# Optimization experiments

Hardware: AMD Instinct MI355X
Metric: run time of the kernel (lower is better)

Reference implementation:

```python
import jax, jax.numpy as jnp
import numpy as np

B, L, D, H = 2, 2048, 1024, 16
HD = D // H  # head_dim = 64


def setup_inputs() -> dict:
    key = jax.random.key(0)
    ks = jax.random.split(key, 8)
    queries = jax.random.normal(ks[0], (B, L, D), dtype=jnp.float32)
    keys = jax.random.normal(ks[1], (B, L, D), dtype=jnp.float32)
    values = jax.random.normal(ks[2], (B, L, D), dtype=jnp.float32)
    mask = jax.random.randint(ks[3], (B, L, L), 0, 2) > 0  # True = masked
    s = 1.0 / np.sqrt(D)
    W_q = jax.random.normal(ks[4], (D, D), dtype=jnp.float32) * s
    W_k = jax.random.normal(ks[5], (D, D), dtype=jnp.float32) * s
    W_v = jax.random.normal(ks[6], (D, D), dtype=jnp.float32) * s
    W_o = jax.random.normal(ks[7], (D, D), dtype=jnp.float32) * s
    return {"queries": queries, "keys": keys, "values": values,
            "W_q": W_q, "W_k": W_k, "W_v": W_v, "W_o": W_o, "mask": mask}


def _split_heads(x):
    # [B, L, D] -> [B, H, L, HD]
    return x.reshape(B, L, H, HD).transpose(0, 2, 1, 3)


def reference(queries, keys, values, W_q, W_k, W_v, W_o, mask):
    # Linear projections (nn.Linear: x @ W.T, no bias)
    q = _split_heads(queries @ W_q.T)   # [B,H,Lq,HD]
    k = _split_heads(keys @ W_k.T)      # [B,H,Lk,HD]
    v = _split_heads(values @ W_v.T)    # [B,H,Lk,HD]
    scores = jnp.einsum('bnqd,bnkd->bnqk', q, k) / np.sqrt(HD)
    scores = jnp.where(mask[:, None, :, :], -1e9, scores)
    attn = jax.nn.softmax(scores, axis=-1)
    ctx = jnp.einsum('bnqk,bnkd->bnqd', attn, v)
    ctx = ctx.transpose(0, 2, 1, 3).reshape(B, L, D)
    return ctx @ W_o.T  # dropout p=0.0 -> identity
```

## Files before the change

kernel.cpp:

```cpp
#include <hip/hip_runtime.h>
#include <hip/hip_bf16.h>

typedef __bf16 bf16;
typedef __attribute__((ext_vector_type(8))) __bf16 bf16x8;
typedef __attribute__((ext_vector_type(4))) __bf16 bf16x4;
typedef __attribute__((ext_vector_type(4))) float f32x4;

#define B_   2
#define L_   2048
#define D_   1024
#define H_   16
#define HD_  64

__device__ __forceinline__ void gll16(const bf16* g, bf16* l) {
  __builtin_amdgcn_global_load_lds((const __attribute__((address_space(1))) void*)g,
                                   (__attribute__((address_space(3))) void*)l,
                                   16, 0, 0);
}

__global__ void detect_kernel(const unsigned short* __restrict__ q_u,
                              const unsigned char* __restrict__ m_u,
                              int* __restrict__ flags) {
  __shared__ int cnt, odd;
  if (threadIdx.x == 0) { cnt = 0; odd = 0; }
  __syncthreads();
  int c = 0, o = 0;
  for (int i = 0; i < 32; i++) {
    int idx = threadIdx.x * 32 + i;
    unsigned e = (q_u[idx] >> 7) & 0xFF;
    if (e >= 0x8F || (e > 0 && e <= 0x6F)) c++;
    if ((idx & 3) && m_u[idx]) o = 1;
  }
  atomicAdd(&cnt, c);
  if (o) atomicOr(&odd, 1);
  __syncthreads();
  if (threadIdx.x == 0) { flags[0] = (cnt > 512) ? 1 : 0; flags[1] = odd; }
}

__device__ __forceinline__ void canon_body(const void* src, bf16* dst, int i, int f) {
  if (f) {
    const float4* s = (const float4*)src;
    float4 a = s[i / 4], b2 = s[i / 4 + 1];
    bf16x8 o;
    o[0] = (bf16)a.x;  o[1] = (bf16)a.y;  o[2] = (bf16)a.z;  o[3] = (bf16)a.w;
    o[4] = (bf16)b2.x; o[5] = (bf16)b2.y; o[6] = (bf16)b2.z; o[7] = (bf16)b2.w;
    *(bf16x8*)(dst + i) = o;
  } else {
    *(bf16x8*)(dst + i) = ((const bf16x8*)src)[i / 8];
  }
}

__global__ __launch_bounds__(256) void canon_all(
    const void* xq, const void* xk, const void* xv,
    const void* Wq, const void* Wk, const void* Wv, const void* Wo,
    bf16* cxq, bf16* cxk, bf16* cxv,
    bf16* cWq, bf16* cWk, bf16* cWv, bf16* cWo,
    const int* __restrict__ flags) {
  const int f = flags[0];
  int t = blockIdx.x;
  const void* src; bf16* dst; int base;
  if (t < 2048)      { src = xq; dst = cxq; base = t * 2048; }
  else if (t < 4096) { src = xk; dst = cxk; base = (t - 2048) * 2048; }
  else if (t < 6144) { src = xv; dst = cxv; base = (t - 4096) * 2048; }
  else {
    int w = t - 6144, wi = w >> 9;
    base = (w & 511) * 2048;
    if (wi == 0)      { src = Wq; dst = cWq; }
    else if (wi == 1) { src = Wk; dst = cWk; }
    else if (wi == 2) { src = Wv; dst = cWv; }
    else              { src = Wo; dst = cWo; }
  }
  canon_body(src, dst, base + threadIdx.x * 8, f);
}

__global__ __launch_bounds__(256) void pack_mask(const void* __restrict__ mp,
                                                 const int* __restrict__ flags,
                                                 unsigned* __restrict__ bitsT) {
  int wid = blockIdx.x * 256 + threadIdx.x;
  unsigned v = 0;
  if (flags[1]) {
    const uchar4* p = (const uchar4*)mp;
#pragma unroll
    for (int c = 0; c < 8; c++) {
      uchar4 u = p[wid * 8 + c];
      v |= (u.x ? 1u : 0u) << (c * 4 + 0);
      v |= (u.y ? 1u : 0u) << (c * 4 + 1);
      v |= (u.z ? 1u : 0u) << (c * 4 + 2);
      v |= (u.w ? 1u : 0u) << (c * 4 + 3);
    }
  } else {
    const int4* p = (const int4*)mp;
#pragma unroll
    for (int c = 0; c < 8; c++) {
      int4 u = p[wid * 8 + c];
      v |= (u.x ? 1u : 0u) << (c * 4 + 0);
      v |= (u.y ? 1u : 0u) << (c * 4 + 1);
      v |= (u.z ? 1u : 0u) << (c * 4 + 2);
      v |= (u.w ? 1u : 0u) << (c * 4 + 3);
    }
  }
  int row = wid >> 6, word = wid & 63;
  int kt = word >> 1, half = word & 1;
  bitsT[((size_t)kt * 4096 + row) * 2 + half] = v;
}

__global__ __launch_bounds__(256) void gemm_qkv(
    const bf16* __restrict__ Aq, const bf16* __restrict__ Bq, bf16* __restrict__ Cq,
    const bf16* __restrict__ Ak, const bf16* __restrict__ Bk, bf16* __restrict__ Ck,
    const bf16* __restrict__ Av, const bf16* __restrict__ Bv, bf16* __restrict__ VT) {
  __shared__ bf16 smem[64 * 136];
  bf16* sA = smem;
  bf16* sB = smem + 4096;
  const int z = blockIdx.z;
  const bf16* A  = (z == 0) ? Aq : (z == 1) ? Ak : Av;
  const bf16* Bm = (z == 0) ? Bq : (z == 1) ? Bk : Bv;

  const int tid = threadIdx.x;
  const int w = tid >> 6, lane = tid & 63, qd = lane >> 4, r = lane & 15;
  const int wm = w >> 1, wn = w & 1;
  const int m0 = blockIdx.x * 128, n0 = blockIdx.y * 64;

  f32x4 acc[4][2];
#pragma unroll
  for (int i = 0; i < 4; i++)
#pragma unroll
    for (int j = 0; j < 2; j++) acc[i][j] = (f32x4){0.f, 0.f, 0.f, 0.f};

  for (int k0 = 0; k0 < 1024; k0 += 32) {
    __syncthreads();
    {
      int c0 = tid;
      gll16(A + (size_t)(m0 + (c0 >> 2)) * 1024 + k0 + (c0 & 3) * 8, sA + c0 * 8);
      int c1 = 256 + tid;
      gll16(A + (size_t)(m0 + (c1 >> 2)) * 1024 + k0 + (c1 & 3) * 8, sA + c1 * 8);
      int cb = tid;
      gll16(Bm + (size_t)(n0 + (cb >> 2)) * 1024 + k0 + (cb & 3) * 8, sB + cb * 8);
    }
    __syncthreads();
    bf16x8 af[4], bfv[2];
#pragma unroll
    for (int i = 0; i < 4; i++)
      af[i] = *(const bf16x8*)&sA[(wm * 64 + i * 16 + r) * 32 + qd * 8];
#pragma unroll
    for (int j = 0; j < 2; j++)
      bfv[j] = *(const bf16x8*)&sB[(wn * 32 + j * 16 + r) * 32 + qd * 8];
#pragma unroll
    for (int i = 0; i < 4; i++)
#pragma unroll
      for (int j = 0; j < 2; j++)
        acc[i][j] = __builtin_amdgcn_mfma_f32_16x16x32_bf16(af[i], bfv[j], acc[i][j], 0, 0, 0);
  }

  if (z < 2) {
    bf16* C = (z == 0) ? Cq : Ck;
#pragma unroll
    for (int i = 0; i < 4; i++)
#pragma unroll
      for (int j = 0; j < 2; j++)
#pragma unroll
        for (int rr = 0; rr < 4; rr++) {
          int row = m0 + wm * 64 + i * 16 + qd * 4 + rr;
          int col = n0 + wn * 32 + j * 16 + r;
          C[(size_t)row * 1024 + col] = (bf16)acc[i][j][rr];
        }
  } else {
    __syncthreads();
#pragma unroll
    for (int i = 0; i < 4; i++)
#pragma unroll
      for (int j = 0; j < 2; j++) {
        int col = wn * 32 + j * 16 + r;
        int rowb = wm * 64 + i * 16 + qd * 4;
        bf16x4 v4;
#pragma unroll
        for (int rr = 0; rr < 4; rr++) v4[rr] = (bf16)acc[i][j][rr];
        *(bf16x4*)&smem[col * 136 + rowb] = v4;
      }
    __syncthreads();
    const int b = m0 >> 11, tok0 = m0 & 2047, h = n0 >> 6;
    const int bh = b * 16 + h;
#pragma unroll
    for (int p = 0; p < 4; p++) {
      int c = p * 256 + tid;
      int d = c >> 4, ch = c & 15;
      bf16x8 v = *(const bf16x8*)&smem[d * 136 + ch * 8];
      *(bf16x8*)(VT + ((size_t)(bh * 64 + d)) * 2048 + tok0 + ch * 8) = v;
    }
  }
}

__global__ __launch_bounds__(256) void gemm_nt_out(const bf16* __restrict__ A,
                                                   const bf16* __restrict__ Bm,
                                                   void* __restrict__ Cout,
                                                   const int* __restrict__ flags) {
  __shared__ bf16 sA[128 * 32];
  __shared__ bf16 sB[64 * 32];
  const int tid = threadIdx.x;
  const int w = tid >> 6, lane = tid & 63, qd = lane >> 4, r = lane & 15;
  const int wm = w >> 1, wn = w & 1;
  const int m0 = blockIdx.x * 128, n0 = blockIdx.y * 64;

  f32x4 acc[4][2];
#pragma unroll
  for (int i = 0; i < 4; i++)
#pragma unroll
    for (int j = 0; j < 2; j++) acc[i][j] = (f32x4){0.f, 0.f, 0.f, 0.f};

  for (int k0 = 0; k0 < 1024; k0 += 32) {
    __syncthreads();
    {
      int c0 = tid;
      gll16(A + (size_t)(m0 + (c0 >> 2)) * 1024 + k0 + (c0 & 3) * 8, sA + c0 * 8);
      int c1 = 256 + tid;
      gll16(A + (size_t)(m0 + (c1 >> 2)) * 1024 + k0 + (c1 & 3) * 8, sA + c1 * 8);
      int cb = tid;
      gll16(Bm + (size_t)(n0 + (cb >> 2)) * 1024 + k0 + (cb & 3) * 8, sB + cb * 8);
    }
    __syncthreads();
    bf16x8 af[4], bfv[2];
#pragma unroll
    for (int i = 0; i < 4; i++)
      af[i] = *(const bf16x8*)&sA[(wm * 64 + i * 16 + r) * 32 + qd * 8];
#pragma unroll
    for (int j = 0; j < 2; j++)
      bfv[j] = *(const bf16x8*)&sB[(wn * 32 + j * 16 + r) * 32 + qd * 8];
#pragma unroll
    for (int i = 0; i < 4; i++)
#pragma unroll
      for (int j = 0; j < 2; j++)
        acc[i][j] = __builtin_amdgcn_mfma_f32_16x16x32_bf16(af[i], bfv[j], acc[i][j], 0, 0, 0);
  }
  const int f = flags[0];
#pragma unroll
  for (int i = 0; i < 4; i++)
#pragma unroll
    for (int j = 0; j < 2; j++)
#pragma unroll
      for (int rr = 0; rr < 4; rr++) {
        int row = m0 + wm * 64 + i * 16 + qd * 4 + rr;
        int col = n0 + wn * 32 + j * 16 + r;
        if (f) ((float*)Cout)[(size_t)row * 1024 + col] = acc[i][j][rr];
        else   ((bf16*)Cout)[(size_t)row * 1024 + col] = (bf16)acc[i][j][rr];
      }
}

__global__ __launch_bounds__(256) void attn_kernel(const bf16* __restrict__ Q,
                                                   const bf16* __restrict__ Kp,
                                                   const bf16* __restrict__ Vt,
                                                   const unsigned* __restrict__ bitsT,
                                                   bf16* __restrict__ CTX) {
  __shared__ bf16 sK[64 * 64];
  __shared__ bf16 sVT[64 * 64];
  __shared__ bf16 sP[128 * 72];
  const int tid = threadIdx.x;
  const int w = tid >> 6, lane = tid & 63, qd = lane >> 4, r = lane & 15;
  const int bh = blockIdx.y, b = bh >> 4, h = bh & 15;
  const int q0 = blockIdx.x * 128;

  bf16x8 qf[2][2];
#pragma unroll
  for (int i = 0; i < 2; i++)
#pragma unroll
    for (int ks = 0; ks < 2; ks++)
      qf[i][ks] = *(const bf16x8*)(Q + (size_t)(b * L_ + q0 + w * 32 + i * 16 + r) * D_ +
                                   h * HD_ + ks * 32 + qd * 8);

  bf16x8 ones;
#pragma unroll
  for (int e = 0; e < 8; e++) ones[e] = (bf16)1.0f;

  f32x4 o[2][4], lacc[2];
#pragma unroll
  for (int i = 0; i < 2; i++) {
#pragma unroll
    for (int dj = 0; dj < 4; dj++) o[i][dj] = (f32x4){0.f, 0.f, 0.f, 0.f};
    lacc[i] = (f32x4){0.f, 0.f, 0.f, 0.f};
  }

  for (int kt = 0; kt < L_ / 64; kt++) {
    __syncthreads();
#pragma unroll
    for (int p = 0; p < 2; p++) {
      int c = p * 256 + tid;
      int row = c >> 3, kc = c & 7;
      int kcg = kc ^ (row & 7);
      gll16(Kp + (size_t)(b * L_ + kt * 64 + row) * D_ + h * HD_ + kcg * 8, sK + c * 8);
    }
#pragma unroll
    for (int p = 0; p < 2; p++) {
      int c = p * 256 + tid;
      int row = c >> 3, kc = c & 7;
      int kcg = kc ^ (row & 7);
      gll16(Vt + (size_t)(bh * 64 + row) * L_ + kt * 64 + kcg * 8, sVT + c * 8);
    }
    __syncthreads();

    uint4 mq[2][2];
#pragma unroll
    for (int i = 0; i < 2; i++) {
      const uint4* mp4 = (const uint4*)(bitsT +
          ((size_t)kt * 4096 + b * 2048 + q0 + w * 32 + i * 16 + qd * 4) * 2);
      mq[i][0] = mp4[0];
      mq[i][1] = mp4[1];
    }

    bf16x8 kf[4][2];
#pragma unroll
    for (int j = 0; j < 4; j++)
#pragma unroll
      for (int ks = 0; ks < 2; ks++) {
        int row = j * 16 + r;
        int phys = (ks * 4 + qd) ^ (row & 7);
        kf[j][ks] = *(const bf16x8*)&sK[row * 64 + phys * 8];
      }

#pragma unroll
    for (int i = 0; i < 2; i++) {
      f32x4 S[4];
#pragma unroll
      for (int j = 0; j < 4; j++) {
        S[j] = (f32x4){0.f, 0.f, 0.f, 0.f};
#pragma unroll
        for (int ks = 0; ks < 2; ks++)
          S[j] = __builtin_amdgcn_mfma_f32_16x16x32_bf16(qf[i][ks], kf[j][ks], S[j], 0, 0, 0);
      }
#pragma unroll
      for (int j = 0; j < 4; j++)
#pragma unroll
        for (int rr = 0; rr < 4; rr++) {
          unsigned w32;
          if (rr == 0) w32 = (j < 2) ? mq[i][0].x : mq[i][0].y;
          else if (rr == 1) w32 = (j < 2) ? mq[i][0].z : mq[i][0].w;
          else if (rr == 2) w32 = (j < 2) ? mq[i][1].x : mq[i][1].y;
          else w32 = (j < 2) ? mq[i][1].z : mq[i][1].w;
          float e = __expf(S[j][rr] * 0.125f);
          bool msk = (w32 >> ((j & 1) * 16 + r)) & 1u;
          sP[(w * 32 + i * 16 + qd * 4 + rr) * 72 + j * 16 + r] = (bf16)(msk ? 0.f : e);
        }
    }
    asm volatile("s_waitcnt lgkmcnt(0)" ::: "memory");

    bf16x8 vf[4][2];
#pragma unroll
    for (int dj = 0; dj < 4; dj++)
#pragma unroll
      for (int ks = 0; ks < 2; ks++) {
        int row = dj * 16 + r;
        int phys = (ks * 4 + qd) ^ (row & 7);
        vf[dj][ks] = *(const bf16x8*)&sVT[row * 64 + phys * 8];
      }
#pragma unroll
    for (int i = 0; i < 2; i++)
#pragma unroll
      for (int ks = 0; ks < 2; ks++) {
        bf16x8 pf = *(const bf16x8*)&sP[(w * 32 + i * 16 + r) * 72 + ks * 32 + qd * 8];
#pragma unroll
        for (int dj = 0; dj < 4; dj++)
          o[i][dj] = __builtin_amdgcn_mfma_f32_16x16x32_bf16(pf, vf[dj][ks], o[i][dj], 0, 0, 0);
        lacc[i] = __builtin_amdgcn_mfma_f32_16x16x32_bf16(pf, ones, lacc[i], 0, 0, 0);
      }
  }

#pragma unroll
  for (int i = 0; i < 2; i++) {
    float inv[4];
#pragma unroll
    for (int rr = 0; rr < 4; rr++) inv[rr] = 1.0f / lacc[i][rr];
#pragma unroll
    for (int dj = 0; dj < 4; dj++)
#pragma unroll
      for (int rr = 0; rr < 4; rr++) {
        int row = b * L_ + q0 + w * 32 + i * 16 + qd * 4 + rr;
        int col = h * HD_ + dj * 16 + r;
        CTX[(size_t)row * D_ + col] = (bf16)(o[i][dj][rr] * inv[rr]);
      }
  }
}

extern "C" void kernel_launch(void* const* d_in, const int* in_sizes, int n_in,
                              void* d_out, int out_size, void* d_ws, size_t ws_size,
                              hipStream_t stream) {
  const void* xq = d_in[0];
  const void* xk = d_in[1];
  const void* xv = d_in[2];
  const void* Wq = d_in[3];
  const void* Wk = d_in[4];
  const void* Wv = d_in[5];
  const void* Wo = d_in[6];
  const void* mask = d_in[7];

  char* ws = (char*)d_ws;
  const size_t MB = 1048576;
  int*      FLAGS = (int*)(ws + 0);
  unsigned* BITS  = (unsigned*)(ws + 4096);
  bf16* cWq = (bf16*)(ws + 2 * MB);
  bf16* cWk = (bf16*)(ws + 4 * MB);
  bf16* cWv = (bf16*)(ws + 6 * MB);
  bf16* cWo = (bf16*)(ws + 8 * MB);
  bf16* cxq = (bf16*)(ws + 10 * MB);
  bf16* cxk = (bf16*)(ws + 18 * MB);
  bf16* cxv = (bf16*)(ws + 26 * MB);
  bf16* Q   = (bf16*)(ws + 34 * MB);
  bf16* K   = (bf16*)(ws + 42 * MB);
  bf16* VT  = (bf16*)(ws + 50 * MB);
  bf16* CTX = cxq;

  detect_kernel<<<1, 256, 0, stream>>>((const unsigned short*)xq,
                                       (const unsigned char*)mask, FLAGS);
  canon_all<<<8192, 256, 0, stream>>>(xq, xk, xv, Wq, Wk, Wv, Wo,
                                      cxq, cxk, cxv, cWq, cWk, cWv, cWo, FLAGS);
  pack_mask<<<1024, 256, 0, stream>>>(mask, FLAGS, BITS);
  gemm_qkv<<<dim3(32, 16, 3), 256, 0, stream>>>(cxq, cWq, Q,
                                                cxk, cWk, K,
                                                cxv, cWv, VT);
  attn_kernel<<<dim3(16, 32), 256, 0, stream>>>(Q, K, VT, BITS, CTX);
  gemm_nt_out<<<dim3(32, 16), 256, 0, stream>>>(CTX, cWo, d_out, FLAGS);
}
```

Before: 285.6 us.

## Split attention over key range, widen GEMM tiles, fold softmax scale into Q

The attention kernel is split into two key halves via a grid z dimension, writing unnormalized partial outputs and row sums that a new combine kernel adds and normalizes. This doubles the number of attention blocks for more parallelism, at the cost of an extra kernel and extra memory traffic. The QKV and output GEMMs move from 128x64 to 128x128 tiles for more reuse per block. The 1/8 scale and log2(e) factor are folded into Q at projection time so the softmax can use a raw exp2. There is no running max, which is safe only if the scores stay bounded.

```diff
diff --git a/kernel.cpp b/kernel.cpp
--- a/kernel.cpp
+++ b/kernel.cpp
@@ -11,6 +11,18 @@
 #define D_   1024
 #define H_   16
 #define HD_  64
+
+__device__ __forceinline__ float fast_exp2(float x) {
+#if defined(__has_builtin)
+#if __has_builtin(__builtin_amdgcn_exp2f)
+  return __builtin_amdgcn_exp2f(x);
+#else
+  float e; asm("v_exp_f32 %0, %1" : "=v"(e) : "v"(x)); return e;
+#endif
+#else
+  float e; asm("v_exp_f32 %0, %1" : "=v"(e) : "v"(x)); return e;
+#endif
+}
 
 __device__ __forceinline__ void gll16(const bf16* g, bf16* l) {
   __builtin_amdgcn_global_load_lds((const __attribute__((address_space(1))) void*)g,
@@ -108,7 +120,7 @@
     const bf16* __restrict__ Aq, const bf16* __restrict__ Bq, bf16* __restrict__ Cq,
     const bf16* __restrict__ Ak, const bf16* __restrict__ Bk, bf16* __restrict__ Ck,
     const bf16* __restrict__ Av, const bf16* __restrict__ Bv, bf16* __restrict__ VT) {
-  __shared__ bf16 smem[64 * 136];
+  __shared__ bf16 smem[128 * 136];
   bf16* sA = smem;
   bf16* sB = smem + 4096;
   const int z = blockIdx.z;
@@ -118,58 +130,61 @@
   const int tid = threadIdx.x;
   const int w = tid >> 6, lane = tid & 63, qd = lane >> 4, r = lane & 15;
   const int wm = w >> 1, wn = w & 1;
-  const int m0 = blockIdx.x * 128, n0 = blockIdx.y * 64;
-
-  f32x4 acc[4][2];
+  const int m0 = blockIdx.x * 128, n0 = blockIdx.y * 128;
+
+  f32x4 acc[4][4];
 #pragma unroll
   for (int i = 0; i < 4; i++)
 #pragma unroll
-    for (int j = 0; j < 2; j++) acc[i][j] = (f32x4){0.f, 0.f, 0.f, 0.f};
+    for (int j = 0; j < 4; j++) acc[i][j] = (f32x4){0.f, 0.f, 0.f, 0.f};
 
   for (int k0 = 0; k0 < 1024; k0 += 32) {
     __syncthreads();
-    {
-      int c0 = tid;
-      gll16(A + (size_t)(m0 + (c0 >> 2)) * 1024 + k0 + (c0 & 3) * 8, sA + c0 * 8);
-      int c1 = 256 + tid;
-      gll16(A + (size_t)(m0 + (c1 >> 2)) * 1024 + k0 + (c1 & 3) * 8, sA + c1 * 8);
-      int cb = tid;
-      gll16(Bm + (size_t)(n0 + (cb >> 2)) * 1024 + k0 + (cb & 3) * 8, sB + cb * 8);
-    }
-    __syncthreads();
-    bf16x8 af[4], bfv[2];
+#pragma unroll
+    for (int p = 0; p < 2; p++) {
+      int c = p * 256 + tid;
+      gll16(A + (size_t)(m0 + (c >> 2)) * 1024 + k0 + (c & 3) * 8, sA + c * 8);
+    }
+#pragma unroll
+    for (int p = 0; p < 2; p++) {
+      int c = p * 256 + tid;
+      gll16(Bm + (size_t)(n0 + (c >> 2)) * 1024 + k0 + (c & 3) * 8, sB + c * 8);
+    }
+    __syncthreads();
+    bf16x8 af[4], bfv[4];
 #pragma unroll
     for (int i = 0; i < 4; i++)
       af[i] = *(const bf16x8*)&sA[(wm * 64 + i * 16 + r) * 32 + qd * 8];
 #pragma unroll
-    for (int j = 0; j < 2; j++)
-      bfv[j] = *(const bf16x8*)&sB[(wn * 32 + j * 16 + r) * 32 + qd * 8];
-#pragma unroll
-    for (int i = 0; i < 4; i++)
-#pragma unroll
-      for (int j = 0; j < 2; j++)
+    for (int j = 0; j < 4; j++)
+      bfv[j] = *(const bf16x8*)&sB[(wn * 64 + j * 16 + r) * 32 + qd * 8];
+#pragma unroll
+    for (int i = 0; i < 4; i++)
+#pragma unroll
+      for (int j = 0; j < 4; j++)
         acc[i][j] = __builtin_amdgcn_mfma_f32_16x16x32_bf16(af[i], bfv[j], acc[i][j], 0, 0, 0);
   }
 
   if (z < 2) {
     bf16* C = (z == 0) ? Cq : Ck;
-#pragma unroll
-    for (int i = 0; i < 4; i++)
-#pragma unroll
-      for (int j = 0; j < 2; j++)
+    const float s = (z == 0) ? 0.1803368801f : 1.0f;
+#pragma unroll
+    for (int i = 0; i < 4; i++)
+#pragma unroll
+      for (int j = 0; j < 4; j++)
 #pragma unroll
         for (int rr = 0; rr < 4; rr++) {
           int row = m0 + wm * 64 + i * 16 + qd * 4 + rr;
-          int col = n0 + wn * 32 + j * 16 + r;
-          C[(size_t)row * 1024 + col] = (bf16)acc[i][j][rr];
+          int col = n0 + wn * 64 + j * 16 + r;
+          C[(size_t)row * 1024 + col] = (bf16)(acc[i][j][rr] * s);
         }
   } else {
     __syncthreads();
 #pragma unroll
     for (int i = 0; i < 4; i++)
 #pragma unroll
-      for (int j = 0; j < 2; j++) {
-        int col = wn * 32 + j * 16 + r;
+      for (int j = 0; j < 4; j++) {
+        int col = wn * 64 + j * 16 + r;
         int rowb = wm * 64 + i * 16 + qd * 4;
         bf16x4 v4;
 #pragma unroll
@@ -177,14 +192,14 @@
         *(bf16x4*)&smem[col * 136 + rowb] = v4;
       }
     __syncthreads();
-    const int b = m0 >> 11, tok0 = m0 & 2047, h = n0 >> 6;
-    const int bh = b * 16 + h;
-#pragma unroll
-    for (int p = 0; p < 4; p++) {
-      int c = p * 256 + tid;
-      int d = c >> 4, ch = c & 15;
-      bf16x8 v = *(const bf16x8*)&smem[d * 136 + ch * 8];
-      *(bf16x8*)(VT + ((size_t)(bh * 64 + d)) * 2048 + tok0 + ch * 8) = v;
+    const int b = m0 >> 11, tok0 = m0 & 2047, h0 = n0 >> 6;
+#pragma unroll
+    for (int p = 0; p < 8; p++) {
+      int c = p * 256 + tid;
+      int dl = c >> 4, ch = c & 15;
+      bf16x8 v = *(const bf16x8*)&smem[dl * 136 + ch * 8];
+      int head = h0 + (dl >> 6), d = dl & 63;
+      *(bf16x8*)(VT + ((size_t)((b * 16 + head) * 64 + d)) * 2048 + tok0 + ch * 8) = v;
     }
   }
 }
@@ -194,51 +209,53 @@
                                                    void* __restrict__ Cout,
                                                    const int* __restrict__ flags) {
   __shared__ bf16 sA[128 * 32];
-  __shared__ bf16 sB[64 * 32];
+  __shared__ bf16 sB[128 * 32];
   const int tid = threadIdx.x;
   const int w = tid >> 6, lane = tid & 63, qd = lane >> 4, r = lane & 15;
   const int wm = w >> 1, wn = w & 1;
-  const int m0 = blockIdx.x * 128, n0 = blockIdx.y * 64;
-
-  f32x4 acc[4][2];
+  const int m0 = blockIdx.x * 128, n0 = blockIdx.y * 128;
+
+  f32x4 acc[4][4];
 #pragma unroll
   for (int i = 0; i < 4; i++)
 #pragma unroll
-    for (int j = 0; j < 2; j++) acc[i][j] = (f32x4){0.f, 0.f, 0.f, 0.f};
+    for (int j = 0; j < 4; j++) acc[i][j] = (f32x4){0.f, 0.f, 0.f, 0.f};
 
   for (int k0 = 0; k0 < 1024; k0 += 32) {
     __syncthreads();
-    {
-      int c0 = tid;
-      gll16(A + (size_t)(m0 + (c0 >> 2)) * 1024 + k0 + (c0 & 3) * 8, sA + c0 * 8);
-      int c1 = 256 + tid;
-      gll16(A + (size_t)(m0 + (c1 >> 2)) * 1024 + k0 + (c1 & 3) * 8, sA + c1 * 8);
-      int cb = tid;
-      gll16(Bm + (size_t)(n0 + (cb >> 2)) * 1024 + k0 + (cb & 3) * 8, sB + cb * 8);
-    }
-    __syncthreads();
-    bf16x8 af[4], bfv[2];
+#pragma unroll
+    for (int p = 0; p < 2; p++) {
+      int c = p * 256 + tid;
+      gll16(A + (size_t)(m0 + (c >> 2)) * 1024 + k0 + (c & 3) * 8, sA + c * 8);
+    }
+#pragma unroll
+    for (int p = 0; p < 2; p++) {
+      int c = p * 256 + tid;
+      gll16(Bm + (size_t)(n0 + (c >> 2)) * 1024 + k0 + (c & 3) * 8, sB + c * 8);
+    }
+    __syncthreads();
+    bf16x8 af[4], bfv[4];
 #pragma unroll
     for (int i = 0; i < 4; i++)
       af[i] = *(const bf16x8*)&sA[(wm * 64 + i * 16 + r) * 32 + qd * 8];
 #pragma unroll
-    for (int j = 0; j < 2; j++)
-      bfv[j] = *(const bf16x8*)&sB[(wn * 32 + j * 16 + r) * 32 + qd * 8];
-#pragma unroll
-    for (int i = 0; i < 4; i++)
-#pragma unroll
-      for (int j = 0; j < 2; j++)
+    for (int j = 0; j < 4; j++)
+      bfv[j] = *(const bf16x8*)&sB[(wn * 64 + j * 16 + r) * 32 + qd * 8];
+#pragma unroll
+    for (int i = 0; i < 4; i++)
+#pragma unroll
+      for (int j = 0; j < 4; j++)
         acc[i][j] = __builtin_amdgcn_mfma_f32_16x16x32_bf16(af[i], bfv[j], acc[i][j], 0, 0, 0);
   }
   const int f = flags[0];
 #pragma unroll
   for (int i = 0; i < 4; i++)
 #pragma unroll
-    for (int j = 0; j < 2; j++)
+    for (int j = 0; j < 4; j++)
 #pragma unroll
       for (int rr = 0; rr < 4; rr++) {
         int row = m0 + wm * 64 + i * 16 + qd * 4 + rr;
-        int col = n0 + wn * 32 + j * 16 + r;
+        int col = n0 + wn * 64 + j * 16 + r;
         if (f) ((float*)Cout)[(size_t)row * 1024 + col] = acc[i][j][rr];
         else   ((bf16*)Cout)[(size_t)row * 1024 + col] = (bf16)acc[i][j][rr];
       }
@@ -248,7 +265,8 @@
                                                    const bf16* __restrict__ Kp,
                                                    const bf16* __restrict__ Vt,
                                                    const unsigned* __restrict__ bitsT,
-                                                   bf16* __restrict__ CTX) {
+                                                   bf16* __restrict__ OP,
+                                                   float* __restrict__ LP) {
   __shared__ bf16 sK[64 * 64];
   __shared__ bf16 sVT[64 * 64];
   __shared__ bf16 sP[128 * 72];
@@ -256,6 +274,7 @@
   const int w = tid >> 6, lane = tid & 63, qd = lane >> 4, r = lane & 15;
   const int bh = blockIdx.y, b = bh >> 4, h = bh & 15;
   const int q0 = blockIdx.x * 128;
+  const int z = blockIdx.z;
 
   bf16x8 qf[2][2];
 #pragma unroll
@@ -277,7 +296,7 @@
     lacc[i] = (f32x4){0.f, 0.f, 0.f, 0.f};
   }
 
-  for (int kt = 0; kt < L_ / 64; kt++) {
+  for (int kt = z * 16; kt < z * 16 + 16; kt++) {
     __syncthreads();
 #pragma unroll
     for (int p = 0; p < 2; p++) {
@@ -333,7 +352,7 @@
           else if (rr == 1) w32 = (j < 2) ? mq[i][0].z : mq[i][0].w;
           else if (rr == 2) w32 = (j < 2) ? mq[i][1].x : mq[i][1].y;
           else w32 = (j < 2) ? mq[i][1].z : mq[i][1].w;
-          float e = __expf(S[j][rr] * 0.125f);
+          float e = fast_exp2(S[j][rr]);
           bool msk = (w32 >> ((j & 1) * 16 + r)) & 1u;
           sP[(w * 32 + i * 16 + qd * 4 + rr) * 72 + j * 16 + r] = (bf16)(msk ? 0.f : e);
         }
@@ -363,18 +382,38 @@
 
 #pragma unroll
   for (int i = 0; i < 2; i++) {
-    float inv[4];
-#pragma unroll
-    for (int rr = 0; rr < 4; rr++) inv[rr] = 1.0f / lacc[i][rr];
 #pragma unroll
     for (int dj = 0; dj < 4; dj++)
 #pragma unroll
       for (int rr = 0; rr < 4; rr++) {
-        int row = b * L_ + q0 + w * 32 + i * 16 + qd * 4 + rr;
+        int rg = b * L_ + q0 + w * 32 + i * 16 + qd * 4 + rr;
         int col = h * HD_ + dj * 16 + r;
-        CTX[(size_t)row * D_ + col] = (bf16)(o[i][dj][rr] * inv[rr]);
-      }
-  }
+        OP[((size_t)z * 4096 + rg) * 1024 + col] = (bf16)o[i][dj][rr];
+      }
+    if (r == 0) {
+#pragma unroll
+      for (int rr = 0; rr < 4; rr++) {
+        int rg = b * L_ + q0 + w * 32 + i * 16 + qd * 4 + rr;
+        LP[((size_t)z * 4096 + rg) * 16 + h] = lacc[i][rr];
+      }
+    }
+  }
+}
+
+__global__ __launch_bounds__(256) void combine_kernel(const bf16* __restrict__ OP,
+                                                      const float* __restrict__ LP,
+                                                      bf16* __restrict__ CTX) {
+  size_t idx = ((size_t)blockIdx.x * 256 + threadIdx.x) * 8;
+  int row = (int)(idx >> 10), col = (int)(idx & 1023);
+  bf16x8 a = *(const bf16x8*)(OP + idx);
+  bf16x8 c = *(const bf16x8*)(OP + (size_t)4096 * 1024 + idx);
+  int h = col >> 6;
+  float l = LP[row * 16 + h] + LP[65536 + row * 16 + h];
+  float inv = 1.0f / l;
+  bf16x8 o;
+#pragma unroll
+  for (int e = 0; e < 8; e++) o[e] = (bf16)(((float)a[e] + (float)c[e]) * inv);
+  *(bf16x8*)(CTX + idx) = o;
 }
 
 extern "C" void kernel_launch(void* const* d_in, const int* in_sizes, int n_in,
@@ -393,26 +432,29 @@
   const size_t MB = 1048576;
   int*      FLAGS = (int*)(ws + 0);
   unsigned* BITS  = (unsigned*)(ws + 4096);
-  bf16* cWq = (bf16*)(ws + 2 * MB);
-  bf16* cWk = (bf16*)(ws + 4 * MB);
-  bf16* cWv = (bf16*)(ws + 6 * MB);
-  bf16* cWo = (bf16*)(ws + 8 * MB);
+  bf16* cWo = (bf16*)(ws + 2 * MB);
+  bf16* cWq = (bf16*)(ws + 4 * MB);
+  bf16* cWk = (bf16*)(ws + 6 * MB);
+  bf16* cWv = (bf16*)(ws + 8 * MB);
   bf16* cxq = (bf16*)(ws + 10 * MB);
   bf16* cxk = (bf16*)(ws + 18 * MB);
   bf16* cxv = (bf16*)(ws + 26 * MB);
   bf16* Q   = (bf16*)(ws + 34 * MB);
   bf16* K   = (bf16*)(ws + 42 * MB);
   bf16* VT  = (bf16*)(ws + 50 * MB);
-  bf16* CTX = cxq;
+  bf16*  OP  = (bf16*)(ws + 4 * MB);
+  float* LP  = (float*)(ws + 20 * MB);
+  bf16*  CTX = (bf16*)(ws + 26 * MB);
 
   detect_kernel<<<1, 256, 0, stream>>>((const unsigned short*)xq,
                                        (const unsigned char*)mask, FLAGS);
   canon_all<<<8192, 256, 0, stream>>>(xq, xk, xv, Wq, Wk, Wv, Wo,
                                       cxq, cxk, cxv, cWq, cWk, cWv, cWo, FLAGS);
   pack_mask<<<1024, 256, 0, stream>>>(mask, FLAGS, BITS);
-  gemm_qkv<<<dim3(32, 16, 3), 256, 0, stream>>>(cxq, cWq, Q,
-                                                cxk, cWk, K,
-                                                cxv, cWv, VT);
-  attn_kernel<<<dim3(16, 32), 256, 0, stream>>>(Q, K, VT, BITS, CTX);
-  gemm_nt_out<<<dim3(32, 16), 256, 0, stream>>>(CTX, cWo, d_out, FLAGS);
-}
+  gemm_qkv<<<dim3(32, 8, 3), 256, 0, stream>>>(cxq, cWq, Q,
+                                               cxk, cWk, K,
+                                               cxv, cWv, VT);
+  attn_kernel<<<dim3(16, 32, 2), 256, 0, stream>>>(Q, K, VT, BITS, OP, LP);
+  combine_kernel<<<2048, 256, 0, stream>>>(OP, LP, CTX);
+  gemm_nt_out<<<dim3(32, 8), 256, 0, stream>>>(CTX, cWo, d_out, FLAGS);
+}
```

New measurement: 280.5 us. No clear change (-1.8%).
